# Performance work log

Hardware: AMD Instinct MI355X
Metric: run time of the kernel (lower is better)

The kernel has to match this reference:

```python
import jax, jax.numpy as jnp
import numpy as np

N = 20000
E = 320000
D = 256
OUT = 256
NEG_SLOPE = 0.2


def setup_inputs() -> dict:
    key = jax.random.key(0)
    ks = jax.random.split(key, 16)
    s = 1.0 / np.sqrt(D)
    x = jax.random.normal(ks[0], (N, D), dtype=jnp.float32)
    edge_index = jax.random.randint(ks[1], (2, E), 0, N, dtype=jnp.int64)
    W1 = jax.random.uniform(ks[2], (D, D), jnp.float32, -s, s)
    W2 = jax.random.uniform(ks[3], (D, D), jnp.float32, -s, s)
    Ws = jax.random.uniform(ks[4], (6, D, D), jnp.float32, -s, s)      # per-layer GATConv lin weight
    a_src = jax.random.uniform(ks[5], (6, D), jnp.float32, -s, s)      # per-layer att_src
    a_dst = jax.random.uniform(ks[6], (6, D), jnp.float32, -s, s)      # per-layer att_dst
    bias = jnp.zeros((6, D), dtype=jnp.float32)                        # per-layer GATConv bias
    W3 = jax.random.uniform(ks[7], (2 * D, OUT), jnp.float32, -s, s)
    return {"x": x, "edge_index": edge_index, "W1": W1, "W2": W2,
            "Ws": Ws, "a_src": a_src, "a_dst": a_dst, "bias": bias, "W3": W3}


def _gat_layer(h, src, dst, W, asrc, adst, b):
    # h: [N, D] -> linear transform
    hw = h @ W                                         # [N, D]
    e_src = hw @ asrc                                  # [N]
    e_dst = hw @ adst                                  # [N]
    e = jax.nn.leaky_relu(e_src[src] + e_dst[dst], NEG_SLOPE)  # [E]
    # softmax over incoming edges per destination node
    m = jax.ops.segment_max(e, dst, num_segments=N)    # [N], -inf for empty segs (unused)
    ee = jnp.exp(e - m[dst])                           # [E]
    denom = jax.ops.segment_sum(ee, dst, num_segments=N)
    alpha = ee / denom[dst]                            # [E]
    msg = alpha[:, None] * hw[src]                     # [E, D]
    out = jax.ops.segment_sum(msg, dst, num_segments=N)  # [N, D]
    return out + b


def reference(x, edge_index, W1, W2, Ws, a_src, a_dst, bias, W3):
    src, dst = edge_index[0], edge_index[1]
    h = x @ W1
    h = h @ W2
    for i in range(6):
        h = _gat_layer(h, src, dst, Ws[i], a_src[i], a_dst[i], bias[i])
    h = jnp.concatenate((h, h), axis=1)   # [N, 2D]
    h = jax.nn.relu(h)
    return h @ W3                          # [N, OUT]
```

## Files before the change

### kernel.cpp

```cpp
#include <hip/hip_runtime.h>
#include <hip/hip_fp16.h>
#include <stdint.h>

#define NNODES 20000
#define EEDGES 320000
#define DD     256
#define NEG_SLOPE 0.2f
#define SCAN_BLOCKS ((NNODES + 255) / 256)

typedef _Float16 half8 __attribute__((ext_vector_type(8)));
typedef _Float16 half4 __attribute__((ext_vector_type(4)));
typedef float f32x4 __attribute__((ext_vector_type(4)));


__global__ void zero_ints_k(int* __restrict__ p, int n) {
    int i = blockIdx.x * 256 + threadIdx.x;
    if (i < n) p[i] = 0;
}

__global__ void hist_k(const int* __restrict__ dst, int* __restrict__ rowptr) {
    int i = blockIdx.x * 256 + threadIdx.x;
    if (i < EEDGES) atomicAdd(&rowptr[dst[i] + 1], 1);
}

__global__ __launch_bounds__(256) void scan1_k(int* __restrict__ rowptr, int* __restrict__ bsums) {
    __shared__ int buf[256];
    int idx = blockIdx.x * 256 + threadIdx.x;
    int v = (idx < NNODES) ? rowptr[idx + 1] : 0;
    buf[threadIdx.x] = v;
    __syncthreads();
#pragma unroll
    for (int off = 1; off < 256; off <<= 1) {
        int t = (threadIdx.x >= (unsigned)off) ? buf[threadIdx.x - off] : 0;
        __syncthreads();
        buf[threadIdx.x] += t;
        __syncthreads();
    }
    if (idx < NNODES) rowptr[idx + 1] = buf[threadIdx.x];
    if (threadIdx.x == 255) bsums[blockIdx.x] = buf[255];
}

__global__ __launch_bounds__(128) void scan2_k(int* __restrict__ bsums) {
    __shared__ int buf[128];
    int v = (threadIdx.x < SCAN_BLOCKS) ? bsums[threadIdx.x] : 0;
    buf[threadIdx.x] = v;
    __syncthreads();
#pragma unroll
    for (int off = 1; off < 128; off <<= 1) {
        int t = (threadIdx.x >= (unsigned)off) ? buf[threadIdx.x - off] : 0;
        __syncthreads();
        buf[threadIdx.x] += t;
        __syncthreads();
    }
    if (threadIdx.x < SCAN_BLOCKS) bsums[threadIdx.x] = buf[threadIdx.x];
}

__global__ void scan3_k(int* __restrict__ rowptr, const int* __restrict__ bsums,
                        int* __restrict__ cursor) {
    int idx = blockIdx.x * 256 + threadIdx.x;
    if (idx < NNODES) {
        int v = rowptr[idx + 1];
        if (blockIdx.x > 0) { v += bsums[blockIdx.x - 1]; rowptr[idx + 1] = v; }
        if (idx + 1 < NNODES) cursor[idx + 1] = v;
        if (idx == 0) cursor[0] = 0;
    }
}

__global__ void scatter_k(const int* __restrict__ src, const int* __restrict__ dst,
                          int* __restrict__ cursor, int* __restrict__ colsrc) {
    int i = blockIdx.x * 256 + threadIdx.x;
    if (i < EEDGES) {
        int d = dst[i];
        int pos = atomicAdd(&cursor[d], 1);
        colsrc[pos] = src[i];
    }
}


__global__ void cvt_split_k(const float* __restrict__ X, _Float16* __restrict__ Xh,
                            _Float16* __restrict__ Xl, int n) {
    int i = blockIdx.x * 256 + threadIdx.x;
    if (i < n) {
        float v = X[i];
        _Float16 hi = (_Float16)v;
        Xh[i] = hi;
        Xl[i] = (_Float16)(v - (float)hi);
    }
}


template<bool SUM>
__global__ void cvt_w_k(const float* __restrict__ W, _Float16* __restrict__ Wh,
                        _Float16* __restrict__ Wl) {
    int i = blockIdx.x * 256 + threadIdx.x;
    if (i < DD * DD) {
        int k = i >> 8, n = i & 255;
        float v = W[i];
        if (SUM) v += W[i + DD * DD];
        _Float16 hi = (_Float16)v;
        Wh[n * DD + k] = hi;
        Wl[n * DD + k] = (_Float16)(v - (float)hi);
    }
}


template<bool OUT_SPLIT>
__global__ __launch_bounds__(256) void gemm16_k(
    const _Float16* __restrict__ Ah, const _Float16* __restrict__ Al,
    const _Float16* __restrict__ Bh, const _Float16* __restrict__ Bl,
    float* __restrict__ C, _Float16* __restrict__ Ch, _Float16* __restrict__ Cl, int M)
{
    __shared__ _Float16 As_h[64][40], As_l[64][40], Bs_h[64][40], Bs_l[64][40];
    const int t = threadIdx.x;
    const int lane = t & 63;
    const int w = t >> 6;
    const int rowBase = blockIdx.y * 64;
    const int colBase = blockIdx.x * 64;
    const int mo = (w & 1) * 32;
    const int no = (w >> 1) * 32;

    const int srow = t >> 2;
    const int sseg = (t & 3) * 8;
    const int garow = rowBase + srow;
    const size_t aoff = (size_t)garow * DD + sseg;
    const size_t boff = (size_t)(colBase + srow) * DD + sseg;

    f32x4 acc00 = {0.f,0.f,0.f,0.f}, acc01 = acc00, acc10 = acc00, acc11 = acc00;
    const int4 zero4 = make_int4(0, 0, 0, 0);
    int4 ra_h, ra_l, rb_h, rb_l;

    ra_h = (garow < M) ? *(const int4*)(Ah + aoff) : zero4;
    ra_l = (garow < M) ? *(const int4*)(Al + aoff) : zero4;
    rb_h = *(const int4*)(Bh + boff);
    rb_l = *(const int4*)(Bl + boff);

    for (int s = 0; s < 8; ++s) {
        __syncthreads();
        *(int4*)&As_h[srow][sseg] = ra_h;
        *(int4*)&As_l[srow][sseg] = ra_l;
        *(int4*)&Bs_h[srow][sseg] = rb_h;
        *(int4*)&Bs_l[srow][sseg] = rb_l;
        __syncthreads();

        if (s < 7) {
            int kn = (s + 1) * 32;
            ra_h = (garow < M) ? *(const int4*)(Ah + aoff + kn) : zero4;
            ra_l = (garow < M) ? *(const int4*)(Al + aoff + kn) : zero4;
            rb_h = *(const int4*)(Bh + boff + kn);
            rb_l = *(const int4*)(Bl + boff + kn);
        }

        const int fr = lane & 15;
        const int fq = (lane >> 4) * 8;
        half8 a0h = *(const half8*)&As_h[mo + fr     ][fq];
        half8 a1h = *(const half8*)&As_h[mo + 16 + fr][fq];
        half8 a0l = *(const half8*)&As_l[mo + fr     ][fq];
        half8 a1l = *(const half8*)&As_l[mo + 16 + fr][fq];
        half8 b0h = *(const half8*)&Bs_h[no + fr     ][fq];
        half8 b1h = *(const half8*)&Bs_h[no + 16 + fr][fq];
        half8 b0l = *(const half8*)&Bs_l[no + fr     ][fq];
        half8 b1l = *(const half8*)&Bs_l[no + 16 + fr][fq];

        acc00 = __builtin_amdgcn_mfma_f32_16x16x32_f16(a0h, b0h, acc00, 0, 0, 0);
        acc01 = __builtin_amdgcn_mfma_f32_16x16x32_f16(a0h, b1h, acc01, 0, 0, 0);
        acc10 = __builtin_amdgcn_mfma_f32_16x16x32_f16(a1h, b0h, acc10, 0, 0, 0);
        acc11 = __builtin_amdgcn_mfma_f32_16x16x32_f16(a1h, b1h, acc11, 0, 0, 0);
        acc00 = __builtin_amdgcn_mfma_f32_16x16x32_f16(a0h, b0l, acc00, 0, 0, 0);
        acc01 = __builtin_amdgcn_mfma_f32_16x16x32_f16(a0h, b1l, acc01, 0, 0, 0);
        acc10 = __builtin_amdgcn_mfma_f32_16x16x32_f16(a1h, b0l, acc10, 0, 0, 0);
        acc11 = __builtin_amdgcn_mfma_f32_16x16x32_f16(a1h, b1l, acc11, 0, 0, 0);
        acc00 = __builtin_amdgcn_mfma_f32_16x16x32_f16(a0l, b0h, acc00, 0, 0, 0);
        acc01 = __builtin_amdgcn_mfma_f32_16x16x32_f16(a0l, b1h, acc01, 0, 0, 0);
        acc10 = __builtin_amdgcn_mfma_f32_16x16x32_f16(a1l, b0h, acc10, 0, 0, 0);
        acc11 = __builtin_amdgcn_mfma_f32_16x16x32_f16(a1l, b1h, acc11, 0, 0, 0);
        acc00 = __builtin_amdgcn_mfma_f32_16x16x32_f16(a0l, b0l, acc00, 0, 0, 0);
        acc01 = __builtin_amdgcn_mfma_f32_16x16x32_f16(a0l, b1l, acc01, 0, 0, 0);
        acc10 = __builtin_amdgcn_mfma_f32_16x16x32_f16(a1l, b0l, acc10, 0, 0, 0);
        acc11 = __builtin_amdgcn_mfma_f32_16x16x32_f16(a1l, b1l, acc11, 0, 0, 0);
    }

    const int ccol = lane & 15;
    const int crq = (lane >> 4) * 4;
#define EPI(ACC, MI, NI) \
    _Pragma("unroll") \
    for (int r = 0; r < 4; ++r) { \
        int grow = rowBase + mo + 16 * MI + crq + r; \
        if (grow < M) { \
            int gcol = colBase + no + 16 * NI + ccol; \
            float v = ACC[r]; \
            if (OUT_SPLIT) { \
                _Float16 hi = (_Float16)v; \
                Ch[(size_t)grow * DD + gcol] = hi; \
                Cl[(size_t)grow * DD + gcol] = (_Float16)(v - (float)hi); \
            } else { \
                C[(size_t)grow * DD + gcol] = v; \
            } \
        } \
    }
    EPI(acc00, 0, 0) EPI(acc01, 0, 1) EPI(acc10, 1, 0) EPI(acc11, 1, 1)
#undef EPI
}


__global__ __launch_bounds__(256) void dots_k(const float* __restrict__ hw,
                                              const float* __restrict__ asrc,
                                              const float* __restrict__ adst,
                                              float* __restrict__ es, float* __restrict__ ed) {
    int wave = threadIdx.x >> 6;
    int lane = threadIdx.x & 63;
    int node = blockIdx.x * 4 + wave;
    if (node >= NNODES) return;
    float4 v = *(const float4*)(hw + (size_t)node * DD + lane * 4);
    float4 a = *(const float4*)(asrc + lane * 4);
    float4 b = *(const float4*)(adst + lane * 4);
    float s = v.x * a.x + v.y * a.y + v.z * a.z + v.w * a.w;
    float d = v.x * b.x + v.y * b.y + v.z * b.z + v.w * b.w;
#pragma unroll
    for (int off = 32; off; off >>= 1) {
        s += __shfl_xor(s, off);
        d += __shfl_xor(d, off);
    }
    if (lane == 0) { es[node] = s; ed[node] = d; }
}


template<bool RELU>
__global__ __launch_bounds__(256) void gat_agg_k(const float* __restrict__ hw,
                                                 const float* __restrict__ es,
                                                 const float* __restrict__ ed,
                                                 const int* __restrict__ rowptr,
                                                 const int* __restrict__ colsrc,
                                                 float* __restrict__ ealpha,
                                                 const float* __restrict__ bias,
                                                 _Float16* __restrict__ hh,
                                                 _Float16* __restrict__ hl) {
    int wave = threadIdx.x >> 6;
    int lane = threadIdx.x & 63;
    int node = blockIdx.x * 4 + wave;
    if (node >= NNODES) return;
    int start = rowptr[node], end = rowptr[node + 1];
    int deg = end - start;
    float edd = ed[node];

    float4 acc0 = make_float4(0.f, 0.f, 0.f, 0.f);
    float4 acc1 = acc0, acc2 = acc0, acc3 = acc0;
    float4 acc4 = acc0, acc5 = acc0, acc6 = acc0, acc7 = acc0;

#define FMA4(ACC, W, V) \
    ACC.x = fmaf(W, V.x, ACC.x); ACC.y = fmaf(W, V.y, ACC.y); \
    ACC.z = fmaf(W, V.z, ACC.z); ACC.w = fmaf(W, V.w, ACC.w);

    if (deg <= 64) {
        if (deg > 0) {
            int j = start + lane;
            bool valid = j < end;
            int msrc = valid ? colsrc[j] : 0;
            float e = valid ? es[msrc] + edd : -INFINITY;
            e = fmaxf(e, NEG_SLOPE * e);
            float mx = e;
#pragma unroll
            for (int off = 32; off; off >>= 1) mx = fmaxf(mx, __shfl_xor(mx, off));
            float ee = valid ? expf(e - mx) : 0.f;
            float sum = ee;
#pragma unroll
            for (int off = 32; off; off >>= 1) sum += __shfl_xor(sum, off);
            float w = ee / sum;

            int j2 = 0;
            for (; j2 + 8 <= deg; j2 += 8) {
                int s0 = __shfl(msrc, j2 + 0), s1 = __shfl(msrc, j2 + 1);
                int s2 = __shfl(msrc, j2 + 2), s3 = __shfl(msrc, j2 + 3);
                int s4 = __shfl(msrc, j2 + 4), s5 = __shfl(msrc, j2 + 5);
                int s6 = __shfl(msrc, j2 + 6), s7 = __shfl(msrc, j2 + 7);
                float w0 = __shfl(w, j2 + 0), w1 = __shfl(w, j2 + 1);
                float w2 = __shfl(w, j2 + 2), w3 = __shfl(w, j2 + 3);
                float w4 = __shfl(w, j2 + 4), w5 = __shfl(w, j2 + 5);
                float w6 = __shfl(w, j2 + 6), w7 = __shfl(w, j2 + 7);
                float4 v0 = *(const float4*)(hw + (size_t)s0 * DD + lane * 4);
                float4 v1 = *(const float4*)(hw + (size_t)s1 * DD + lane * 4);
                float4 v2 = *(const float4*)(hw + (size_t)s2 * DD + lane * 4);
                float4 v3 = *(const float4*)(hw + (size_t)s3 * DD + lane * 4);
                float4 v4 = *(const float4*)(hw + (size_t)s4 * DD + lane * 4);
                float4 v5 = *(const float4*)(hw + (size_t)s5 * DD + lane * 4);
                float4 v6 = *(const float4*)(hw + (size_t)s6 * DD + lane * 4);
                float4 v7 = *(const float4*)(hw + (size_t)s7 * DD + lane * 4);
                FMA4(acc0, w0, v0); FMA4(acc1, w1, v1);
                FMA4(acc2, w2, v2); FMA4(acc3, w3, v3);
                FMA4(acc4, w4, v4); FMA4(acc5, w5, v5);
                FMA4(acc6, w6, v6); FMA4(acc7, w7, v7);
            }
            if (j2 + 4 <= deg) {
                int s0 = __shfl(msrc, j2 + 0), s1 = __shfl(msrc, j2 + 1);
                int s2 = __shfl(msrc, j2 + 2), s3 = __shfl(msrc, j2 + 3);
                float w0 = __shfl(w, j2 + 0), w1 = __shfl(w, j2 + 1);
                float w2 = __shfl(w, j2 + 2), w3 = __shfl(w, j2 + 3);
                float4 v0 = *(const float4*)(hw + (size_t)s0 * DD + lane * 4);
                float4 v1 = *(const float4*)(hw + (size_t)s1 * DD + lane * 4);
                float4 v2 = *(const float4*)(hw + (size_t)s2 * DD + lane * 4);
                float4 v3 = *(const float4*)(hw + (size_t)s3 * DD + lane * 4);
                FMA4(acc0, w0, v0); FMA4(acc1, w1, v1);
                FMA4(acc2, w2, v2); FMA4(acc3, w3, v3);
                j2 += 4;
            }
            for (; j2 < deg; ++j2) {
                int   s0 = __shfl(msrc, j2);
                float w0 = __shfl(w, j2);
                float4 v0 = *(const float4*)(hw + (size_t)s0 * DD + lane * 4);
                FMA4(acc0, w0, v0);
            }
        }
    } else {
        float mx = -INFINITY;
        for (int j = start + lane; j < end; j += 64) {
            float e = es[colsrc[j]] + edd;
            e = fmaxf(e, NEG_SLOPE * e);
            mx = fmaxf(mx, e);
        }
#pragma unroll
        for (int off = 32; off; off >>= 1) mx = fmaxf(mx, __shfl_xor(mx, off));
        float sum = 0.f;
        for (int j = start + lane; j < end; j += 64) {
            float e = es[colsrc[j]] + edd;
            e = fmaxf(e, NEG_SLOPE * e);
            float ee = expf(e - mx);
            ealpha[j] = ee;
            sum += ee;
        }
#pragma unroll
        for (int off = 32; off; off >>= 1) sum += __shfl_xor(sum, off);
        float inv = 1.f / sum;
        int j = start;
        for (; j + 4 <= end; j += 4) {
            int s0 = colsrc[j], s1 = colsrc[j + 1], s2 = colsrc[j + 2], s3 = colsrc[j + 3];
            float w0 = ealpha[j] * inv, w1 = ealpha[j + 1] * inv;
            float w2 = ealpha[j + 2] * inv, w3 = ealpha[j + 3] * inv;
            float4 v0 = *(const float4*)(hw + (size_t)s0 * DD + lane * 4);
            float4 v1 = *(const float4*)(hw + (size_t)s1 * DD + lane * 4);
            float4 v2 = *(const float4*)(hw + (size_t)s2 * DD + lane * 4);
            float4 v3 = *(const float4*)(hw + (size_t)s3 * DD + lane * 4);
            FMA4(acc0, w0, v0); FMA4(acc1, w1, v1);
            FMA4(acc2, w2, v2); FMA4(acc3, w3, v3);
        }
        for (; j < end; ++j) {
            int s0 = colsrc[j];
            float w0 = ealpha[j] * inv;
            float4 v0 = *(const float4*)(hw + (size_t)s0 * DD + lane * 4);
            FMA4(acc0, w0, v0);
        }
    }
#undef FMA4

    acc0.x += acc4.x; acc0.y += acc4.y; acc0.z += acc4.z; acc0.w += acc4.w;
    acc1.x += acc5.x; acc1.y += acc5.y; acc1.z += acc5.z; acc1.w += acc5.w;
    acc2.x += acc6.x; acc2.y += acc6.y; acc2.z += acc6.z; acc2.w += acc6.w;
    acc3.x += acc7.x; acc3.y += acc7.y; acc3.z += acc7.z; acc3.w += acc7.w;
    acc0.x += acc1.x; acc0.y += acc1.y; acc0.z += acc1.z; acc0.w += acc1.w;
    acc2.x += acc3.x; acc2.y += acc3.y; acc2.z += acc3.z; acc2.w += acc3.w;
    acc0.x += acc2.x; acc0.y += acc2.y; acc0.z += acc2.z; acc0.w += acc2.w;
    float4 b4 = *(const float4*)(bias + lane * 4);
    acc0.x += b4.x; acc0.y += b4.y; acc0.z += b4.z; acc0.w += b4.w;
    if (RELU) {
        acc0.x = fmaxf(acc0.x, 0.f); acc0.y = fmaxf(acc0.y, 0.f);
        acc0.z = fmaxf(acc0.z, 0.f); acc0.w = fmaxf(acc0.w, 0.f);
    }
    size_t base = (size_t)node * DD + lane * 4;
    _Float16 h0 = (_Float16)acc0.x, h1 = (_Float16)acc0.y;
    _Float16 h2 = (_Float16)acc0.z, h3 = (_Float16)acc0.w;
    half4 hv; hv[0] = h0; hv[1] = h1; hv[2] = h2; hv[3] = h3;
    half4 lv;
    lv[0] = (_Float16)(acc0.x - (float)h0); lv[1] = (_Float16)(acc0.y - (float)h1);
    lv[2] = (_Float16)(acc0.z - (float)h2); lv[3] = (_Float16)(acc0.w - (float)h3);
    *(half4*)(hh + base) = hv;
    *(half4*)(hl + base) = lv;
}


extern "C" void kernel_launch(void* const* d_in, const int* in_sizes, int n_in,
                              void* d_out, int out_size, void* d_ws, size_t ws_size,
                              hipStream_t stream) {
    const float* x     = (const float*)d_in[0];
    const int*   ei    = (const int*)d_in[1];
    const float* W1    = (const float*)d_in[2];
    const float* W2    = (const float*)d_in[3];
    const float* Ws    = (const float*)d_in[4];
    const float* a_src = (const float*)d_in[5];
    const float* a_dst = (const float*)d_in[6];
    const float* bias  = (const float*)d_in[7];
    const float* W3    = (const float*)d_in[8];
    float* out = (float*)d_out;

    const int* src = ei;
    const int* dst = ei + EEDGES;

    const size_t ND = (size_t)NNODES * DD;

    float* bufA   = (float*)d_ws;
    float* es     = bufA + ND;
    float* edv    = es + NNODES;
    float* ealpha = edv + NNODES;
    int*   rowptr = (int*)(ealpha + EEDGES);
    int*   cursor = rowptr + (NNODES + 1);
    int*   colsrc = cursor + NNODES;
    int*   bsums  = colsrc + EEDGES;
    _Float16* P0h = (_Float16*)(((uintptr_t)(bsums + SCAN_BLOCKS) + 15) & ~(uintptr_t)15);
    _Float16* P0l = P0h + ND;
    _Float16* P1h = P0l + ND;
    _Float16* P1l = P1h + ND;
    _Float16* WT  = P1l + ND;
    const size_t WSZ = (size_t)DD * DD;

    zero_ints_k<<<(NNODES + 1 + 255) / 256, 256, 0, stream>>>(rowptr, NNODES + 1);
    hist_k<<<(EEDGES + 255) / 256, 256, 0, stream>>>(dst, rowptr);
    scan1_k<<<SCAN_BLOCKS, 256, 0, stream>>>(rowptr, bsums);
    scan2_k<<<1, 128, 0, stream>>>(bsums);
    scan3_k<<<SCAN_BLOCKS, 256, 0, stream>>>(rowptr, bsums, cursor);
    scatter_k<<<(EEDGES + 255) / 256, 256, 0, stream>>>(src, dst, cursor, colsrc);

    const int WBLK = (DD * DD + 255) / 256;
    cvt_w_k<false><<<WBLK, 256, 0, stream>>>(W1, WT + 0 * 2 * WSZ, WT + 0 * 2 * WSZ + WSZ);
    cvt_w_k<false><<<WBLK, 256, 0, stream>>>(W2, WT + 1 * 2 * WSZ, WT + 1 * 2 * WSZ + WSZ);
    for (int l = 0; l < 6; ++l)
        cvt_w_k<false><<<WBLK, 256, 0, stream>>>(Ws + (size_t)l * WSZ,
                                                 WT + (2 + l) * 2 * WSZ,
                                                 WT + (2 + l) * 2 * WSZ + WSZ);
    cvt_w_k<true><<<WBLK, 256, 0, stream>>>(W3, WT + 8 * 2 * WSZ, WT + 8 * 2 * WSZ + WSZ);

    cvt_split_k<<<(int)((ND + 255) / 256), 256, 0, stream>>>(x, P0h, P0l, (int)ND);

    dim3 g16(DD / 64, (NNODES + 63) / 64);
    const int nodeBlocks = (NNODES + 3) / 4;

#define WTH(i) (WT + (i) * 2 * WSZ)
#define WTL(i) (WT + (i) * 2 * WSZ + WSZ)

    gemm16_k<true><<<g16, 256, 0, stream>>>(P0h, P0l, WTH(0), WTL(0), nullptr, P1h, P1l, NNODES);
    gemm16_k<true><<<g16, 256, 0, stream>>>(P1h, P1l, WTH(1), WTL(1), nullptr, P0h, P0l, NNODES);

    for (int l = 0; l < 6; ++l) {
        gemm16_k<false><<<g16, 256, 0, stream>>>(P0h, P0l, WTH(2 + l), WTL(2 + l),
                                                 bufA, nullptr, nullptr, NNODES);
        dots_k<<<nodeBlocks, 256, 0, stream>>>(bufA, a_src + (size_t)l * DD,
                                               a_dst + (size_t)l * DD, es, edv);
        if (l < 5)
            gat_agg_k<false><<<nodeBlocks, 256, 0, stream>>>(bufA, es, edv, rowptr, colsrc,
                                                             ealpha, bias + (size_t)l * DD,
                                                             P0h, P0l);
        else
            gat_agg_k<true><<<nodeBlocks, 256, 0, stream>>>(bufA, es, edv, rowptr, colsrc,
                                                            ealpha, bias + (size_t)l * DD,
                                                            P0h, P0l);
    }

    gemm16_k<false><<<g16, 256, 0, stream>>>(P0h, P0l, WTH(8), WTL(8), out,
                                             nullptr, nullptr, NNODES);
#undef WTH
#undef WTL
}
```

Measured before the change: 653.3 us.

## Retile split-fp16 GEMM to 128x128 with swizzled LDS; pipeline GAT gathers

The split-precision MFMA GEMM moves from 64x64 tiles to 128x128 tiles. Each wave now computes a 64x64 sub-tile with a 4x4 accumulator array, K is staged 64 at a time, and the LDS layout is XOR-swizzled so fragment reads avoid bank conflicts. The aim is more MFMA work per shared-memory load and fewer global loads, at the cost of a much smaller grid (314 blocks), heavier register and LDS use, and unguarded A-row loads past M on the last row tile. The GAT aggregation for degree ≤64 now double-buffers gathers of eight neighbour rows with sched_barrier, so the loads for the next batch overlap the FMAs of the current one, and it uses four accumulators instead of eight.

```diff
diff --git a/kernel.cpp b/kernel.cpp
--- a/kernel.cpp
+++ b/kernel.cpp
@@ -105,100 +105,116 @@
 
 
 template<bool OUT_SPLIT>
-__global__ __launch_bounds__(256) void gemm16_k(
+__global__ __launch_bounds__(256, 2) void gemm128_k(
     const _Float16* __restrict__ Ah, const _Float16* __restrict__ Al,
     const _Float16* __restrict__ Bh, const _Float16* __restrict__ Bl,
     float* __restrict__ C, _Float16* __restrict__ Ch, _Float16* __restrict__ Cl, int M)
 {
-    __shared__ _Float16 As_h[64][40], As_l[64][40], Bs_h[64][40], Bs_l[64][40];
+    __shared__ _Float16 sAh[128 * 64], sAl[128 * 64], sBh[128 * 64], sBl[128 * 64];
     const int t = threadIdx.x;
     const int lane = t & 63;
     const int w = t >> 6;
-    const int rowBase = blockIdx.y * 64;
-    const int colBase = blockIdx.x * 64;
-    const int mo = (w & 1) * 32;
-    const int no = (w >> 1) * 32;
-
-    const int srow = t >> 2;
-    const int sseg = (t & 3) * 8;
-    const int garow = rowBase + srow;
-    const size_t aoff = (size_t)garow * DD + sseg;
-    const size_t boff = (size_t)(colBase + srow) * DD + sseg;
-
-    f32x4 acc00 = {0.f,0.f,0.f,0.f}, acc01 = acc00, acc10 = acc00, acc11 = acc00;
-    const int4 zero4 = make_int4(0, 0, 0, 0);
-    int4 ra_h, ra_l, rb_h, rb_l;
-
-    ra_h = (garow < M) ? *(const int4*)(Ah + aoff) : zero4;
-    ra_l = (garow < M) ? *(const int4*)(Al + aoff) : zero4;
-    rb_h = *(const int4*)(Bh + boff);
-    rb_l = *(const int4*)(Bl + boff);
-
-    for (int s = 0; s < 8; ++s) {
-        __syncthreads();
-        *(int4*)&As_h[srow][sseg] = ra_h;
-        *(int4*)&As_l[srow][sseg] = ra_l;
-        *(int4*)&Bs_h[srow][sseg] = rb_h;
-        *(int4*)&Bs_l[srow][sseg] = rb_l;
-        __syncthreads();
-
-        if (s < 7) {
-            int kn = (s + 1) * 32;
-            ra_h = (garow < M) ? *(const int4*)(Ah + aoff + kn) : zero4;
-            ra_l = (garow < M) ? *(const int4*)(Al + aoff + kn) : zero4;
-            rb_h = *(const int4*)(Bh + boff + kn);
-            rb_l = *(const int4*)(Bl + boff + kn);
-        }
-
-        const int fr = lane & 15;
-        const int fq = (lane >> 4) * 8;
-        half8 a0h = *(const half8*)&As_h[mo + fr     ][fq];
-        half8 a1h = *(const half8*)&As_h[mo + 16 + fr][fq];
-        half8 a0l = *(const half8*)&As_l[mo + fr     ][fq];
-        half8 a1l = *(const half8*)&As_l[mo + 16 + fr][fq];
-        half8 b0h = *(const half8*)&Bs_h[no + fr     ][fq];
-        half8 b1h = *(const half8*)&Bs_h[no + 16 + fr][fq];
-        half8 b0l = *(const half8*)&Bs_l[no + fr     ][fq];
-        half8 b1l = *(const half8*)&Bs_l[no + 16 + fr][fq];
-
-        acc00 = __builtin_amdgcn_mfma_f32_16x16x32_f16(a0h, b0h, acc00, 0, 0, 0);
-        acc01 = __builtin_amdgcn_mfma_f32_16x16x32_f16(a0h, b1h, acc01, 0, 0, 0);
-        acc10 = __builtin_amdgcn_mfma_f32_16x16x32_f16(a1h, b0h, acc10, 0, 0, 0);
-        acc11 = __builtin_amdgcn_mfma_f32_16x16x32_f16(a1h, b1h, acc11, 0, 0, 0);
-        acc00 = __builtin_amdgcn_mfma_f32_16x16x32_f16(a0h, b0l, acc00, 0, 0, 0);
-        acc01 = __builtin_amdgcn_mfma_f32_16x16x32_f16(a0h, b1l, acc01, 0, 0, 0);
-        acc10 = __builtin_amdgcn_mfma_f32_16x16x32_f16(a1h, b0l, acc10, 0, 0, 0);
-        acc11 = __builtin_amdgcn_mfma_f32_16x16x32_f16(a1h, b1l, acc11, 0, 0, 0);
-        acc00 = __builtin_amdgcn_mfma_f32_16x16x32_f16(a0l, b0h, acc00, 0, 0, 0);
-        acc01 = __builtin_amdgcn_mfma_f32_16x16x32_f16(a0l, b1h, acc01, 0, 0, 0);
-        acc10 = __builtin_amdgcn_mfma_f32_16x16x32_f16(a1l, b0h, acc10, 0, 0, 0);
-        acc11 = __builtin_amdgcn_mfma_f32_16x16x32_f16(a1l, b1h, acc11, 0, 0, 0);
-        acc00 = __builtin_amdgcn_mfma_f32_16x16x32_f16(a0l, b0l, acc00, 0, 0, 0);
-        acc01 = __builtin_amdgcn_mfma_f32_16x16x32_f16(a0l, b1l, acc01, 0, 0, 0);
-        acc10 = __builtin_amdgcn_mfma_f32_16x16x32_f16(a1l, b0l, acc10, 0, 0, 0);
-        acc11 = __builtin_amdgcn_mfma_f32_16x16x32_f16(a1l, b1l, acc11, 0, 0, 0);
-    }
+    const int rowBase = blockIdx.y * 128;
+    const int colBase = blockIdx.x * 128;
+    const int mo = (w & 1) * 64;
+    const int no = (w >> 1) * 64;
+
+    const int srow0 = t >> 3;
+    const int ss8   = (t & 7) * 8;
+    const int ds8   = ((t & 7) ^ (srow0 & 7)) * 8;
+
+    f32x4 acc[4][4];
+#pragma unroll
+    for (int m = 0; m < 4; ++m)
+#pragma unroll
+        for (int n = 0; n < 4; ++n) acc[m][n] = (f32x4){0.f, 0.f, 0.f, 0.f};
+
+    int4 pa_h[4], pa_l[4], pb_h[4], pb_l[4];
+
+#define LOADSTAGE(S) \
+    _Pragma("unroll") \
+    for (int i = 0; i < 4; ++i) { \
+        int row = i * 32 + srow0; \
+        size_t aoff = (size_t)(rowBase + row) * DD + (S) * 64 + ss8; \
+        size_t boff = (size_t)(colBase + row) * DD + (S) * 64 + ss8; \
+        pa_h[i] = *(const int4*)(Ah + aoff); \
+        pa_l[i] = *(const int4*)(Al + aoff); \
+        pb_h[i] = *(const int4*)(Bh + boff); \
+        pb_l[i] = *(const int4*)(Bl + boff); \
+    }
+
+#define WRITESTAGE() \
+    _Pragma("unroll") \
+    for (int i = 0; i < 4; ++i) { \
+        int lo = (i * 32 + srow0) * 64 + ds8; \
+        *(int4*)(sAh + lo) = pa_h[i]; \
+        *(int4*)(sAl + lo) = pa_l[i]; \
+        *(int4*)(sBh + lo) = pb_h[i]; \
+        *(int4*)(sBl + lo) = pb_l[i]; \
+    }
+
+    LOADSTAGE(0);
+    const int fr = lane & 15;
+    const int fq = lane >> 4;
+
+    for (int s = 0; s < 4; ++s) {
+        __syncthreads();
+        WRITESTAGE();
+        __syncthreads();
+        if (s < 3) { LOADSTAGE(s + 1); }
+
+#pragma unroll
+        for (int kk = 0; kk < 2; ++kk) {
+            half8 ah[4], al[4], bh[4], bl[4];
+#pragma unroll
+            for (int m = 0; m < 4; ++m) {
+                int ra = mo + m * 16 + fr;
+                int oa = ra * 64 + (((kk * 4 + fq) ^ (ra & 7)) << 3);
+                ah[m] = *(const half8*)(sAh + oa);
+                al[m] = *(const half8*)(sAl + oa);
+                int rb = no + m * 16 + fr;
+                int ob = rb * 64 + (((kk * 4 + fq) ^ (rb & 7)) << 3);
+                bh[m] = *(const half8*)(sBh + ob);
+                bl[m] = *(const half8*)(sBl + ob);
+            }
+#pragma unroll
+            for (int m = 0; m < 4; ++m)
+#pragma unroll
+                for (int n = 0; n < 4; ++n) {
+                    acc[m][n] = __builtin_amdgcn_mfma_f32_16x16x32_f16(ah[m], bh[n], acc[m][n], 0, 0, 0);
+                    acc[m][n] = __builtin_amdgcn_mfma_f32_16x16x32_f16(ah[m], bl[n], acc[m][n], 0, 0, 0);
+                    acc[m][n] = __builtin_amdgcn_mfma_f32_16x16x32_f16(al[m], bh[n], acc[m][n], 0, 0, 0);
+                    acc[m][n] = __builtin_amdgcn_mfma_f32_16x16x32_f16(al[m], bl[n], acc[m][n], 0, 0, 0);
+                }
+        }
+    }
+#undef LOADSTAGE
+#undef WRITESTAGE
 
     const int ccol = lane & 15;
     const int crq = (lane >> 4) * 4;
-#define EPI(ACC, MI, NI) \
-    _Pragma("unroll") \
-    for (int r = 0; r < 4; ++r) { \
-        int grow = rowBase + mo + 16 * MI + crq + r; \
-        if (grow < M) { \
-            int gcol = colBase + no + 16 * NI + ccol; \
-            float v = ACC[r]; \
-            if (OUT_SPLIT) { \
-                _Float16 hi = (_Float16)v; \
-                Ch[(size_t)grow * DD + gcol] = hi; \
-                Cl[(size_t)grow * DD + gcol] = (_Float16)(v - (float)hi); \
-            } else { \
-                C[(size_t)grow * DD + gcol] = v; \
-            } \
-        } \
-    }
-    EPI(acc00, 0, 0) EPI(acc01, 0, 1) EPI(acc10, 1, 0) EPI(acc11, 1, 1)
-#undef EPI
+#pragma unroll
+    for (int m = 0; m < 4; ++m) {
+        int growb = rowBase + mo + m * 16 + crq;
+#pragma unroll
+        for (int n = 0; n < 4; ++n) {
+            int gcol = colBase + no + n * 16 + ccol;
+#pragma unroll
+            for (int r = 0; r < 4; ++r) {
+                int grow = growb + r;
+                if (grow < M) {
+                    float v = acc[m][n][r];
+                    if (OUT_SPLIT) {
+                        _Float16 hi = (_Float16)v;
+                        Ch[(size_t)grow * DD + gcol] = hi;
+                        Cl[(size_t)grow * DD + gcol] = (_Float16)(v - (float)hi);
+                    } else {
+                        C[(size_t)grow * DD + gcol] = v;
+                    }
+                }
+            }
+        }
+    }
 }
 
 
@@ -225,15 +241,15 @@
 
 
 template<bool RELU>
-__global__ __launch_bounds__(256) void gat_agg_k(const float* __restrict__ hw,
-                                                 const float* __restrict__ es,
-                                                 const float* __restrict__ ed,
-                                                 const int* __restrict__ rowptr,
-                                                 const int* __restrict__ colsrc,
-                                                 float* __restrict__ ealpha,
-                                                 const float* __restrict__ bias,
-                                                 _Float16* __restrict__ hh,
-                                                 _Float16* __restrict__ hl) {
+__global__ __launch_bounds__(256, 4) void gat_agg_k(const float* __restrict__ hw,
+                                                    const float* __restrict__ es,
+                                                    const float* __restrict__ ed,
+                                                    const int* __restrict__ rowptr,
+                                                    const int* __restrict__ colsrc,
+                                                    float* __restrict__ ealpha,
+                                                    const float* __restrict__ bias,
+                                                    _Float16* __restrict__ hh,
+                                                    _Float16* __restrict__ hl) {
     int wave = threadIdx.x >> 6;
     int lane = threadIdx.x & 63;
     int node = blockIdx.x * 4 + wave;
@@ -244,72 +260,56 @@
 
     float4 acc0 = make_float4(0.f, 0.f, 0.f, 0.f);
     float4 acc1 = acc0, acc2 = acc0, acc3 = acc0;
-    float4 acc4 = acc0, acc5 = acc0, acc6 = acc0, acc7 = acc0;
-
-#define FMA4(ACC, W, V) \
-    ACC.x = fmaf(W, V.x, ACC.x); ACC.y = fmaf(W, V.y, ACC.y); \
-    ACC.z = fmaf(W, V.z, ACC.z); ACC.w = fmaf(W, V.w, ACC.w);
-
-    if (deg <= 64) {
-        if (deg > 0) {
-            int j = start + lane;
-            bool valid = j < end;
-            int msrc = valid ? colsrc[j] : 0;
-            float e = valid ? es[msrc] + edd : -INFINITY;
-            e = fmaxf(e, NEG_SLOPE * e);
-            float mx = e;
-#pragma unroll
-            for (int off = 32; off; off >>= 1) mx = fmaxf(mx, __shfl_xor(mx, off));
-            float ee = valid ? expf(e - mx) : 0.f;
-            float sum = ee;
-#pragma unroll
-            for (int off = 32; off; off >>= 1) sum += __shfl_xor(sum, off);
-            float w = ee / sum;
-
-            int j2 = 0;
-            for (; j2 + 8 <= deg; j2 += 8) {
-                int s0 = __shfl(msrc, j2 + 0), s1 = __shfl(msrc, j2 + 1);
-                int s2 = __shfl(msrc, j2 + 2), s3 = __shfl(msrc, j2 + 3);
-                int s4 = __shfl(msrc, j2 + 4), s5 = __shfl(msrc, j2 + 5);
-                int s6 = __shfl(msrc, j2 + 6), s7 = __shfl(msrc, j2 + 7);
-                float w0 = __shfl(w, j2 + 0), w1 = __shfl(w, j2 + 1);
-                float w2 = __shfl(w, j2 + 2), w3 = __shfl(w, j2 + 3);
-                float w4 = __shfl(w, j2 + 4), w5 = __shfl(w, j2 + 5);
-                float w6 = __shfl(w, j2 + 6), w7 = __shfl(w, j2 + 7);
-                float4 v0 = *(const float4*)(hw + (size_t)s0 * DD + lane * 4);
-                float4 v1 = *(const float4*)(hw + (size_t)s1 * DD + lane * 4);
-                float4 v2 = *(const float4*)(hw + (size_t)s2 * DD + lane * 4);
-                float4 v3 = *(const float4*)(hw + (size_t)s3 * DD + lane * 4);
-                float4 v4 = *(const float4*)(hw + (size_t)s4 * DD + lane * 4);
-                float4 v5 = *(const float4*)(hw + (size_t)s5 * DD + lane * 4);
-                float4 v6 = *(const float4*)(hw + (size_t)s6 * DD + lane * 4);
-                float4 v7 = *(const float4*)(hw + (size_t)s7 * DD + lane * 4);
-                FMA4(acc0, w0, v0); FMA4(acc1, w1, v1);
-                FMA4(acc2, w2, v2); FMA4(acc3, w3, v3);
-                FMA4(acc4, w4, v4); FMA4(acc5, w5, v5);
-                FMA4(acc6, w6, v6); FMA4(acc7, w7, v7);
-            }
-            if (j2 + 4 <= deg) {
-                int s0 = __shfl(msrc, j2 + 0), s1 = __shfl(msrc, j2 + 1);
-                int s2 = __shfl(msrc, j2 + 2), s3 = __shfl(msrc, j2 + 3);
-                float w0 = __shfl(w, j2 + 0), w1 = __shfl(w, j2 + 1);
-                float w2 = __shfl(w, j2 + 2), w3 = __shfl(w, j2 + 3);
-                float4 v0 = *(const float4*)(hw + (size_t)s0 * DD + lane * 4);
-                float4 v1 = *(const float4*)(hw + (size_t)s1 * DD + lane * 4);
-                float4 v2 = *(const float4*)(hw + (size_t)s2 * DD + lane * 4);
-                float4 v3 = *(const float4*)(hw + (size_t)s3 * DD + lane * 4);
-                FMA4(acc0, w0, v0); FMA4(acc1, w1, v1);
-                FMA4(acc2, w2, v2); FMA4(acc3, w3, v3);
-                j2 += 4;
-            }
-            for (; j2 < deg; ++j2) {
-                int   s0 = __shfl(msrc, j2);
-                float w0 = __shfl(w, j2);
-                float4 v0 = *(const float4*)(hw + (size_t)s0 * DD + lane * 4);
-                FMA4(acc0, w0, v0);
-            }
-        }
-    } else {
+
+#define FMA4(ACC, W_, V) \
+    ACC.x = fmaf(W_, V.x, ACC.x); ACC.y = fmaf(W_, V.y, ACC.y); \
+    ACC.z = fmaf(W_, V.z, ACC.z); ACC.w = fmaf(W_, V.w, ACC.w);
+
+    if (deg > 0 && deg <= 64) {
+        bool valid = lane < deg;
+        int msrc = valid ? colsrc[start + lane] : 0;
+        float e = valid ? es[msrc] + edd : -INFINITY;
+        e = fmaxf(e, NEG_SLOPE * e);
+        float mx = e;
+#pragma unroll
+        for (int off = 32; off; off >>= 1) mx = fmaxf(mx, __shfl_xor(mx, off));
+        float ee = valid ? expf(e - mx) : 0.f;
+        float sum = ee;
+#pragma unroll
+        for (int off = 32; off; off >>= 1) sum += __shfl_xor(sum, off);
+        float w = ee / sum;
+
+#define FETCH8(V, W_, JB) \
+        _Pragma("unroll") \
+        for (int q = 0; q < 8; ++q) { \
+            int sq = __shfl(msrc, (JB) + q); \
+            W_[q] = __shfl(w, (JB) + q); \
+            V[q] = *(const float4*)(hw + (size_t)sq * DD + lane * 4); \
+        }
+
+#define FMA8(V, W_) \
+        FMA4(acc0, W_[0], V[0]); FMA4(acc1, W_[1], V[1]); \
+        FMA4(acc2, W_[2], V[2]); FMA4(acc3, W_[3], V[3]); \
+        FMA4(acc0, W_[4], V[4]); FMA4(acc1, W_[5], V[5]); \
+        FMA4(acc2, W_[6], V[6]); FMA4(acc3, W_[7], V[7]);
+
+        float4 va[8], vb[8];
+        float wa[8], wb[8];
+        FETCH8(va, wa, 0);
+        int jb = 8;
+        for (;;) {
+            if (jb >= deg) { FMA8(va, wa); break; }
+            FETCH8(vb, wb, jb); jb += 8;
+            __builtin_amdgcn_sched_barrier(0);
+            FMA8(va, wa);
+            if (jb >= deg) { FMA8(vb, wb); break; }
+            FETCH8(va, wa, jb); jb += 8;
+            __builtin_amdgcn_sched_barrier(0);
+            FMA8(vb, wb);
+        }
+#undef FETCH8
+#undef FMA8
+    } else if (deg > 64) {
         float mx = -INFINITY;
         for (int j = start + lane; j < end; j += 64) {
             float e = es[colsrc[j]] + edd;
@@ -350,10 +350,6 @@
     }
 #undef FMA4
 
-    acc0.x += acc4.x; acc0.y += acc4.y; acc0.z += acc4.z; acc0.w += acc4.w;
-    acc1.x += acc5.x; acc1.y += acc5.y; acc1.z += acc5.z; acc1.w += acc5.w;
-    acc2.x += acc6.x; acc2.y += acc6.y; acc2.z += acc6.z; acc2.w += acc6.w;
-    acc3.x += acc7.x; acc3.y += acc7.y; acc3.z += acc7.z; acc3.w += acc7.w;
     acc0.x += acc1.x; acc0.y += acc1.y; acc0.z += acc1.z; acc0.w += acc1.w;
     acc2.x += acc3.x; acc2.y += acc3.y; acc2.z += acc3.z; acc2.w += acc3.w;
     acc0.x += acc2.x; acc0.y += acc2.y; acc0.z += acc2.z; acc0.w += acc2.w;
@@ -427,18 +423,18 @@
 
     cvt_split_k<<<(int)((ND + 255) / 256), 256, 0, stream>>>(x, P0h, P0l, (int)ND);
 
-    dim3 g16(DD / 64, (NNODES + 63) / 64);
+    dim3 g128(DD / 128, (NNODES + 127) / 128);
     const int nodeBlocks = (NNODES + 3) / 4;
 
 #define WTH(i) (WT + (i) * 2 * WSZ)
 #define WTL(i) (WT + (i) * 2 * WSZ + WSZ)
 
-    gemm16_k<true><<<g16, 256, 0, stream>>>(P0h, P0l, WTH(0), WTL(0), nullptr, P1h, P1l, NNODES);
-    gemm16_k<true><<<g16, 256, 0, stream>>>(P1h, P1l, WTH(1), WTL(1), nullptr, P0h, P0l, NNODES);
+    gemm128_k<true><<<g128, 256, 0, stream>>>(P0h, P0l, WTH(0), WTL(0), nullptr, P1h, P1l, NNODES);
+    gemm128_k<true><<<g128, 256, 0, stream>>>(P1h, P1l, WTH(1), WTL(1), nullptr, P0h, P0l, NNODES);
 
     for (int l = 0; l < 6; ++l) {
-        gemm16_k<false><<<g16, 256, 0, stream>>>(P0h, P0l, WTH(2 + l), WTL(2 + l),
-                                                 bufA, nullptr, nullptr, NNODES);
+        gemm128_k<false><<<g128, 256, 0, stream>>>(P0h, P0l, WTH(2 + l), WTL(2 + l),
+                                                   bufA, nullptr, nullptr, NNODES);
         dots_k<<<nodeBlocks, 256, 0, stream>>>(bufA, a_src + (size_t)l * DD,
                                                a_dst + (size_t)l * DD, es, edv);
         if (l < 5)
@@ -451,8 +447,8 @@
                                                             P0h, P0l);
     }
 
-    gemm16_k<false><<<g16, 256, 0, stream>>>(P0h, P0l, WTH(8), WTL(8), out,
-                                             nullptr, nullptr, NNODES);
+    gemm128_k<false><<<g128, 256, 0, stream>>>(P0h, P0l, WTH(8), WTL(8), out,
+                                               nullptr, nullptr, NNODES);
 #undef WTH
 #undef WTL
 }
```

Measured after the change: 990.8 us. 1.52x slower.
